# Performance work log

Measured on AMD Instinct MI355X. Metric: run time of the kernel, lower is better.

The kernel has to match this reference:

```python
import jax, jax.numpy as jnp
import numpy as np

N = 4096
W_SCALE = 1.0 / N  # default W_scale = 1/N


def setup_inputs() -> dict:
    key = jax.random.key(0)
    k1, k2 = jax.random.split(key)
    # W: (channels=1, H=512, N=4096), randn * 1/N (default W_scale)
    W = jax.random.normal(k1, (1, 512, N), dtype=jnp.float32) * W_SCALE
    # Lambda_im: omega init -> 2*pi*n/N mod 2*pi; uniform [0, 2pi) stand-in
    Lambda_im = jax.random.uniform(k2, (N,), dtype=jnp.float32) * (2.0 * np.pi)
    return {"W": W, "Lambda_im": Lambda_im, "L": 8192}


def reference(W, Lambda_im, L):
    # version='Lambda_imag_W_real', kernel_to_real='real':
    # K[c,h,l] = sum_n W[c,h,n] * cos(Lambda_im[n] * l)
    pos = jnp.arange(L, dtype=jnp.float32)          # (L,)
    S = jnp.cos(Lambda_im[:, None] * pos[None, :])  # (N, L) Vandermonde-cosine
    K = jnp.einsum("chn,nl->chl", W, S)             # (C, H, L)
    return K
```

## Files before the change

### kernel.cpp

```cpp
#include <hip/hip_runtime.h>
#include <hip/hip_bf16.h>
#include <math.h>


typedef __bf16 bf16_t;
typedef bf16_t bf16x8 __attribute__((ext_vector_type(8)));
typedef float f32x16 __attribute__((ext_vector_type(16)));

#define NK 4096
#define LO 8192
#define BM 128
#define BN 128
#define BK 32
#define LDK 40

__device__ __forceinline__ uint32_t cvt_pk(float lo, float hi) {
    uint32_t r;
    asm("v_cvt_pk_bf16_f32 %0, %1, %2" : "=v"(r) : "v"(lo), "v"(hi));
    return r;
}

__global__ __launch_bounds__(256) void dlr_cosgemm(
    const float* __restrict__ W,
    const float* __restrict__ Lam,
    float* __restrict__ out)
{
    __shared__ uint32_t tbl[NK];
    __shared__ float    cheb[NK];
    __shared__ bf16_t   Al[2][BM][LDK];
    __shared__ bf16_t   Sl[2][BN][LDK];

    const int tid = threadIdx.x;
    const int bid = blockIdx.x;
    const int mt = (bid >> 1) & 3;
    const int nt = ((bid >> 3) << 1) | (bid & 1);
    const int m0 = mt * BM;
    const int n0 = nt * BN;

    for (int i = tid; i < NK; i += 256) {
        double mu = (double)Lam[i] * 0.15915494309189535;
        int a = (int)rint(mu * 8192.0);
        double eps = mu - (double)a * (1.0 / 8192.0);
        int e = (int)rint(eps * 536870912.0);
        e = e > 32767 ? 32767 : (e < -32768 ? -32768 : e);
        tbl[i] = ((uint32_t)a << 16) | ((uint32_t)e & 0xffffu);
        double fr = mu - rint(mu);
        cheb[i] = 2.0f * __builtin_amdgcn_cosf((float)fr);
    }

    const int skk  = (tid & 15) * 2;
    const int srow = (tid >> 4) * 8;
    const int sl0  = n0 + srow;
    const float l29 = (float)sl0 * 0x1p-29f;

    const int arow = tid >> 1;
    const int akh  = (tid & 1) * 16;
    const float* aptr = W + (size_t)(m0 + arow) * NK + akh;

    const int wid = tid >> 6;
    const int lane = tid & 63;
    const int wm = (wid >> 1) * 64;
    const int wn = (wid & 1) * 64;
    const int r31 = lane & 31;
    const int hi8 = (lane >> 5) * 8;

    f32x16 acc[2][2];
    #pragma unroll
    for (int i = 0; i < 2; ++i)
        #pragma unroll
        for (int j = 0; j < 2; ++j)
            #pragma unroll
            for (int r = 0; r < 16; ++r)
                acc[i][j][r] = 0.f;

    __syncthreads();

    auto chain8 = [&](int k, float* c) {
        uint32_t pk = tbl[k];
        float c2 = cheb[k];
        float ef = (float)(int)(short)(pk & 0xffffu);
        uint32_t a = pk >> 16;
        uint32_t prod = a * (uint32_t)sl0;
        float f0 = fmaf((float)(prod & 8191u), 0x1p-13f, ef * l29);
        f0 -= rintf(f0);
        float mu = fmaf((float)a, 0x1p-13f, ef * 0x1p-29f);
        float f1 = f0 + mu; f1 -= rintf(f1);
        c[0] = __builtin_amdgcn_cosf(f0);
        c[1] = __builtin_amdgcn_cosf(f1);
        #pragma unroll
        for (int j = 2; j < 8; ++j) c[j] = fmaf(c2, c[j - 1], -c[j - 2]);
    };

    auto stageS = [&](int buf, int k0) {
        float ca[8], cb[8];
        chain8(k0 + skk, ca);
        chain8(k0 + skk + 1, cb);
        #pragma unroll
        for (int j = 0; j < 8; ++j)
            *(uint32_t*)&Sl[buf][srow + j][skk] = cvt_pk(ca[j], cb[j]);
    };

    auto stageA = [&](int buf, int k0) {
        const float4* g = (const float4*)(aptr + k0);
        float4 v0 = g[0], v1 = g[1], v2 = g[2], v3 = g[3];
        uint4 q0, q1;
        q0.x = cvt_pk(v0.x, v0.y); q0.y = cvt_pk(v0.z, v0.w);
        q0.z = cvt_pk(v1.x, v1.y); q0.w = cvt_pk(v1.z, v1.w);
        q1.x = cvt_pk(v2.x, v2.y); q1.y = cvt_pk(v2.z, v2.w);
        q1.z = cvt_pk(v3.x, v3.y); q1.w = cvt_pk(v3.z, v3.w);
        *(uint4*)&Al[buf][arow][akh]     = q0;
        *(uint4*)&Al[buf][arow][akh + 8] = q1;
    };

    auto compute = [&](int buf) {
        #pragma unroll
        for (int ks = 0; ks < 2; ++ks) {
            const int ko = ks * 16 + hi8;
            bf16x8 a0 = *(const bf16x8*)&Al[buf][wm + r31][ko];
            bf16x8 a1 = *(const bf16x8*)&Al[buf][wm + 32 + r31][ko];
            bf16x8 b0 = *(const bf16x8*)&Sl[buf][wn + r31][ko];
            bf16x8 b1 = *(const bf16x8*)&Sl[buf][wn + 32 + r31][ko];
            acc[0][0] = __builtin_amdgcn_mfma_f32_32x32x16_bf16(a0, b0, acc[0][0], 0, 0, 0);
            acc[0][1] = __builtin_amdgcn_mfma_f32_32x32x16_bf16(a0, b1, acc[0][1], 0, 0, 0);
            acc[1][0] = __builtin_amdgcn_mfma_f32_32x32x16_bf16(a1, b0, acc[1][0], 0, 0, 0);
            acc[1][1] = __builtin_amdgcn_mfma_f32_32x32x16_bf16(a1, b1, acc[1][1], 0, 0, 0);
        }
    };

    stageA(0, 0);
    stageS(0, 0);
    __syncthreads();

    #pragma unroll 2
    for (int it = 0; it < 127; ++it) {
        const int cur = it & 1;
        stageA(cur ^ 1, (it + 1) * BK);
        stageS(cur ^ 1, (it + 1) * BK);
        compute(cur);
        __syncthreads();
    }
    compute(1);

    #pragma unroll
    for (int mi = 0; mi < 2; ++mi) {
        #pragma unroll
        for (int ni = 0; ni < 2; ++ni) {
            const int col = n0 + wn + ni * 32 + r31;
            const int rbase = m0 + wm + mi * 32 + 4 * (lane >> 5);
            #pragma unroll
            for (int reg = 0; reg < 16; ++reg) {
                const int row = rbase + (reg & 3) + 8 * (reg >> 2);
                out[(size_t)row * LO + col] = acc[mi][ni][reg];
            }
        }
    }
}

extern "C" void kernel_launch(void* const* d_in, const int* in_sizes, int n_in,
                              void* d_out, int out_size, void* d_ws, size_t ws_size,
                              hipStream_t stream) {
    const float* W = (const float*)d_in[0];
    const float* Lam = (const float*)d_in[1];
    float* out = (float*)d_out;
    dlr_cosgemm<<<dim3(256), dim3(256), 0, stream>>>(W, Lam, out);
}
```

Measured before the change: 157.0 us.

## Split into prep kernel and split-K 512-thread main GEMM with global A fragments

A prep kernel computes the frequency table and Chebyshev coefficients once and converts W to bf16 in workspace. The main kernel uses 512 threads with an intra-block split-K across two wave groups, BK raised to 64, and A fragments loaded directly from global bf16 into registers with prefetch. Partial sums are reduced through shared memory. This removes the redundant per-block table setup and the A staging through LDS, at the cost of an extra launch, workspace traffic and a reduction epilogue. The original single kernel is kept as a fallback when the workspace is too small.

```diff
diff --git a/kernel.cpp b/kernel.cpp
--- a/kernel.cpp
+++ b/kernel.cpp
@@ -8,11 +8,12 @@
 typedef float f32x16 __attribute__((ext_vector_type(16)));
 
 #define NK 4096
+#define MH 512
 #define LO 8192
 #define BM 128
 #define BN 128
-#define BK 32
-#define LDK 40
+#define BK 64
+#define LDK 72
 
 __device__ __forceinline__ uint32_t cvt_pk(float lo, float hi) {
     uint32_t r;
@@ -20,15 +21,197 @@
     return r;
 }
 
-__global__ __launch_bounds__(256) void dlr_cosgemm(
-    const float* __restrict__ W,
-    const float* __restrict__ Lam,
-    float* __restrict__ out)
+__global__ __launch_bounds__(256) void dlr_prep(
+    const float* __restrict__ W, const float* __restrict__ Lam, void* __restrict__ ws)
+{
+    uint32_t* tbl  = (uint32_t*)ws;
+    float*    cheb = (float*)((char*)ws + NK * 4);
+    bf16_t*   Wb   = (bf16_t*)((char*)ws + NK * 8);
+    const int gid = blockIdx.x * 256 + threadIdx.x;
+    if (gid < NK) {
+        double mu = (double)Lam[gid] * 0.15915494309189535;
+        int a = (int)rint(mu * 8192.0);
+        double eps = mu - (double)a * (1.0 / 8192.0);
+        int e = (int)rint(eps * 536870912.0);
+        e = e > 32767 ? 32767 : (e < -32768 ? -32768 : e);
+        tbl[gid] = ((uint32_t)a << 16) | ((uint32_t)e & 0xffffu);
+        double fr = mu - rint(mu);
+        cheb[gid] = 2.0f * __builtin_amdgcn_cosf((float)fr);
+    }
+    size_t base = (size_t)gid * 8;
+    if (base < (size_t)MH * NK) {
+        const float4* s = (const float4*)(W + base);
+        float4 v0 = s[0], v1 = s[1];
+        uint4 q;
+        q.x = cvt_pk(v0.x, v0.y); q.y = cvt_pk(v0.z, v0.w);
+        q.z = cvt_pk(v1.x, v1.y); q.w = cvt_pk(v1.z, v1.w);
+        *(uint4*)(Wb + base) = q;
+    }
+}
+
+__global__ __launch_bounds__(512, 2) void dlr_main(
+    const void* __restrict__ ws, float* __restrict__ out)
+{
+    const uint32_t* tbl  = (const uint32_t*)ws;
+    const float*    cheb = (const float*)((const char*)ws + NK * 4);
+    const bf16_t*   Wb   = (const bf16_t*)((const char*)ws + NK * 8);
+
+    __shared__ bf16_t Sl[2][BN][LDK];
+    __shared__ float  red[BM][BN + 2];
+
+    const int tid = threadIdx.x;
+    const int bid = blockIdx.x;
+    const int mt = (bid >> 1) & 3;
+    const int nt = ((bid >> 3) << 1) | (bid & 1);
+    const int m0 = mt * BM;
+    const int n0 = nt * BN;
+
+    const int skk  = (tid & 31) * 2;
+    const int srow = (tid >> 5) * 8;
+    const int sl0  = n0 + srow;
+    const float l29 = (float)sl0 * 0x1p-29f;
+
+    const int wid  = tid >> 6;
+    const int lane = tid & 63;
+    const int kg   = wid & 1;
+    const int wn   = ((wid >> 1) & 1) * 64;
+    const int wm   = ((wid >> 2) & 1) * 64;
+    const int r31  = lane & 31;
+    const int hi8  = (lane >> 5) * 8;
+
+    const bf16_t* abase[2][2];
+    #pragma unroll
+    for (int mi = 0; mi < 2; ++mi)
+        #pragma unroll
+        for (int ks = 0; ks < 2; ++ks)
+            abase[mi][ks] = Wb + (size_t)(m0 + wm + mi * 32 + r31) * NK
+                               + kg * 32 + ks * 16 + hi8;
+
+    f32x16 acc[2][2];
+    #pragma unroll
+    for (int i = 0; i < 2; ++i)
+        #pragma unroll
+        for (int j = 0; j < 2; ++j)
+            #pragma unroll
+            for (int r = 0; r < 16; ++r)
+                acc[i][j][r] = 0.f;
+
+    uint32_t tA, tB; float cA, cB;
+    auto loadTbl = [&](int t) {
+        int k = t * BK + skk;
+        tA = tbl[k]; tB = tbl[k + 1];
+        cA = cheb[k]; cB = cheb[k + 1];
+    };
+
+    auto chain8 = [&](uint32_t pk, float c2, float* c) {
+        float ef = (float)(int)(short)(pk & 0xffffu);
+        uint32_t a = pk >> 16;
+        uint32_t prod = a * (uint32_t)sl0;
+        float f0 = fmaf((float)(prod & 8191u), 0x1p-13f, ef * l29);
+        f0 -= rintf(f0);
+        float mu = fmaf((float)a, 0x1p-13f, ef * 0x1p-29f);
+        float f1 = f0 + mu; f1 -= rintf(f1);
+        c[0] = __builtin_amdgcn_cosf(f0);
+        c[1] = __builtin_amdgcn_cosf(f1);
+        #pragma unroll
+        for (int j = 2; j < 8; ++j) c[j] = fmaf(c2, c[j - 1], -c[j - 2]);
+    };
+
+    auto stageS = [&](int buf) {
+        float ca[8], cb[8];
+        chain8(tA, cA, ca);
+        chain8(tB, cB, cb);
+        #pragma unroll
+        for (int j = 0; j < 8; ++j)
+            *(uint32_t*)&Sl[buf][srow + j][skk] = cvt_pk(ca[j], cb[j]);
+    };
+
+    bf16x8 aCur[2][2], aNxt[2][2];
+    auto loadA = [&](bf16x8 a[2][2], int it) {
+        #pragma unroll
+        for (int mi = 0; mi < 2; ++mi)
+            #pragma unroll
+            for (int ks = 0; ks < 2; ++ks)
+                a[mi][ks] = *(const bf16x8*)(abase[mi][ks] + (size_t)it * BK);
+    };
+
+    auto compute = [&](int buf, bf16x8 a[2][2]) {
+        bf16x8 bfr[2][2];
+        #pragma unroll
+        for (int ks = 0; ks < 2; ++ks)
+            #pragma unroll
+            for (int ni = 0; ni < 2; ++ni)
+                bfr[ni][ks] = *(const bf16x8*)&Sl[buf][wn + ni * 32 + r31]
+                                                 [kg * 32 + ks * 16 + hi8];
+        #pragma unroll
+        for (int ks = 0; ks < 2; ++ks)
+            #pragma unroll
+            for (int mi = 0; mi < 2; ++mi)
+                #pragma unroll
+                for (int ni = 0; ni < 2; ++ni)
+                    acc[mi][ni] = __builtin_amdgcn_mfma_f32_32x32x16_bf16(
+                        a[mi][ks], bfr[ni][ks], acc[mi][ni], 0, 0, 0);
+    };
+
+    loadTbl(0);
+    loadA(aCur, 0);
+    stageS(0);
+    loadTbl(1);
+    loadA(aNxt, 0);
+    __syncthreads();
+
+    #pragma unroll 2
+    for (int it = 0; it < 64; ++it) {
+        const int cur = it & 1;
+        if (it < 63) {
+            loadA(aNxt, it + 1);
+            stageS(cur ^ 1);
+        }
+        if (it < 62) loadTbl(it + 2);
+        compute(cur, aCur);
+        #pragma unroll
+        for (int mi = 0; mi < 2; ++mi)
+            #pragma unroll
+            for (int ks = 0; ks < 2; ++ks)
+                aCur[mi][ks] = aNxt[mi][ks];
+        __syncthreads();
+    }
+
+    if (kg == 1) {
+        #pragma unroll
+        for (int mi = 0; mi < 2; ++mi)
+            #pragma unroll
+            for (int ni = 0; ni < 2; ++ni)
+                #pragma unroll
+                for (int rr = 0; rr < 16; ++rr) {
+                    const int row = wm + mi * 32 + (rr & 3) + 8 * (rr >> 2) + 4 * (lane >> 5);
+                    red[row][wn + ni * 32 + r31] = acc[mi][ni][rr];
+                }
+    }
+    __syncthreads();
+    if (kg == 0) {
+        #pragma unroll
+        for (int mi = 0; mi < 2; ++mi)
+            #pragma unroll
+            for (int ni = 0; ni < 2; ++ni) {
+                const int col = n0 + wn + ni * 32 + r31;
+                #pragma unroll
+                for (int rr = 0; rr < 16; ++rr) {
+                    const int row = wm + mi * 32 + (rr & 3) + 8 * (rr >> 2) + 4 * (lane >> 5);
+                    out[(size_t)(m0 + row) * LO + col] =
+                        acc[mi][ni][rr] + red[row][wn + ni * 32 + r31];
+                }
+            }
+    }
+}
+
+__global__ __launch_bounds__(256) void dlr_fb(
+    const float* __restrict__ W, const float* __restrict__ Lam, float* __restrict__ out)
 {
     __shared__ uint32_t tbl[NK];
     __shared__ float    cheb[NK];
-    __shared__ bf16_t   Al[2][BM][LDK];
-    __shared__ bf16_t   Sl[2][BN][LDK];
+    __shared__ bf16_t   Al[2][BM][40];
+    __shared__ bf16_t   Slf[2][BN][40];
 
     const int tid = threadIdx.x;
     const int bid = blockIdx.x;
@@ -52,11 +235,9 @@
     const int srow = (tid >> 4) * 8;
     const int sl0  = n0 + srow;
     const float l29 = (float)sl0 * 0x1p-29f;
-
     const int arow = tid >> 1;
     const int akh  = (tid & 1) * 16;
     const float* aptr = W + (size_t)(m0 + arow) * NK + akh;
-
     const int wid = tid >> 6;
     const int lane = tid & 63;
     const int wm = (wid >> 1) * 64;
@@ -70,9 +251,7 @@
         #pragma unroll
         for (int j = 0; j < 2; ++j)
             #pragma unroll
-            for (int r = 0; r < 16; ++r)
-                acc[i][j][r] = 0.f;
-
+            for (int r = 0; r < 16; ++r) acc[i][j][r] = 0.f;
     __syncthreads();
 
     auto chain8 = [&](int k, float* c) {
@@ -90,16 +269,14 @@
         #pragma unroll
         for (int j = 2; j < 8; ++j) c[j] = fmaf(c2, c[j - 1], -c[j - 2]);
     };
-
     auto stageS = [&](int buf, int k0) {
         float ca[8], cb[8];
         chain8(k0 + skk, ca);
         chain8(k0 + skk + 1, cb);
         #pragma unroll
         for (int j = 0; j < 8; ++j)
-            *(uint32_t*)&Sl[buf][srow + j][skk] = cvt_pk(ca[j], cb[j]);
-    };
-
+            *(uint32_t*)&Slf[buf][srow + j][skk] = cvt_pk(ca[j], cb[j]);
+    };
     auto stageA = [&](int buf, int k0) {
         const float4* g = (const float4*)(aptr + k0);
         float4 v0 = g[0], v1 = g[1], v2 = g[2], v3 = g[3];
@@ -111,15 +288,14 @@
         *(uint4*)&Al[buf][arow][akh]     = q0;
         *(uint4*)&Al[buf][arow][akh + 8] = q1;
     };
-
     auto compute = [&](int buf) {
         #pragma unroll
         for (int ks = 0; ks < 2; ++ks) {
             const int ko = ks * 16 + hi8;
             bf16x8 a0 = *(const bf16x8*)&Al[buf][wm + r31][ko];
             bf16x8 a1 = *(const bf16x8*)&Al[buf][wm + 32 + r31][ko];
-            bf16x8 b0 = *(const bf16x8*)&Sl[buf][wn + r31][ko];
-            bf16x8 b1 = *(const bf16x8*)&Sl[buf][wn + 32 + r31][ko];
+            bf16x8 b0 = *(const bf16x8*)&Slf[buf][wn + r31][ko];
+            bf16x8 b1 = *(const bf16x8*)&Slf[buf][wn + 32 + r31][ko];
             acc[0][0] = __builtin_amdgcn_mfma_f32_32x32x16_bf16(a0, b0, acc[0][0], 0, 0, 0);
             acc[0][1] = __builtin_amdgcn_mfma_f32_32x32x16_bf16(a0, b1, acc[0][1], 0, 0, 0);
             acc[1][0] = __builtin_amdgcn_mfma_f32_32x32x16_bf16(a1, b0, acc[1][0], 0, 0, 0);
@@ -130,19 +306,18 @@
     stageA(0, 0);
     stageS(0, 0);
     __syncthreads();
-
     #pragma unroll 2
     for (int it = 0; it < 127; ++it) {
         const int cur = it & 1;
-        stageA(cur ^ 1, (it + 1) * BK);
-        stageS(cur ^ 1, (it + 1) * BK);
+        stageA(cur ^ 1, (it + 1) * 32);
+        stageS(cur ^ 1, (it + 1) * 32);
         compute(cur);
         __syncthreads();
     }
     compute(1);
 
     #pragma unroll
-    for (int mi = 0; mi < 2; ++mi) {
+    for (int mi = 0; mi < 2; ++mi)
         #pragma unroll
         for (int ni = 0; ni < 2; ++ni) {
             const int col = n0 + wn + ni * 32 + r31;
@@ -153,7 +328,6 @@
                 out[(size_t)row * LO + col] = acc[mi][ni][reg];
             }
         }
-    }
 }
 
 extern "C" void kernel_launch(void* const* d_in, const int* in_sizes, int n_in,
@@ -162,5 +336,11 @@
     const float* W = (const float*)d_in[0];
     const float* Lam = (const float*)d_in[1];
     float* out = (float*)d_out;
-    dlr_cosgemm<<<dim3(256), dim3(256), 0, stream>>>(W, Lam, out);
-}
+    const size_t need = (size_t)NK * 8 + (size_t)MH * NK * 2;
+    if (ws_size >= need) {
+        dlr_prep<<<dim3(1024), dim3(256), 0, stream>>>(W, Lam, d_ws);
+        dlr_main<<<dim3(256), dim3(512), 0, stream>>>(d_ws, out);
+    } else {
+        dlr_fb<<<dim3(256), dim3(256), 0, stream>>>(W, Lam, out);
+    }
+}
```

Result: faster. 132.8 us (-15.4%).

## Split block into producer waves generating cosine tiles and consumer MFMA waves

Applied to the files above, without the earlier changes.

Doubles the block to 512 threads. Four producer waves compute the Chebyshev cosine S-tile into shared memory, while four consumer waves load W directly from global memory into registers, convert it to bf16 and run the MFMAs. BK grows to 64, the A shared-memory tile is removed, A is register-prefetched one step ahead, and s_setprio is raised around the MFMA block. The aim is to overlap the transcendental and VALU work of S generation with matrix-core work. In exchange, each thread holds more registers, and W reads from global memory are strided across rows per lane.

```diff
diff --git a/kernel.cpp b/kernel.cpp
--- a/kernel.cpp
+++ b/kernel.cpp
@@ -8,11 +8,12 @@
 typedef float f32x16 __attribute__((ext_vector_type(16)));
 
 #define NK 4096
+#define MH 512
 #define LO 8192
 #define BM 128
 #define BN 128
-#define BK 32
-#define LDK 40
+#define BK 64
+#define LDK 72
 
 __device__ __forceinline__ uint32_t cvt_pk(float lo, float hi) {
     uint32_t r;
@@ -20,14 +21,13 @@
     return r;
 }
 
-__global__ __launch_bounds__(256) void dlr_cosgemm(
+__global__ __launch_bounds__(512, 2) void dlr_pc(
     const float* __restrict__ W,
     const float* __restrict__ Lam,
     float* __restrict__ out)
 {
     __shared__ uint32_t tbl[NK];
     __shared__ float    cheb[NK];
-    __shared__ bf16_t   Al[2][BM][LDK];
     __shared__ bf16_t   Sl[2][BN][LDK];
 
     const int tid = threadIdx.x;
@@ -37,7 +37,7 @@
     const int m0 = mt * BM;
     const int n0 = nt * BN;
 
-    for (int i = tid; i < NK; i += 256) {
+    for (int i = tid; i < NK; i += 512) {
         double mu = (double)Lam[i] * 0.15915494309189535;
         int a = (int)rint(mu * 8192.0);
         double eps = mu - (double)a * (1.0 / 8192.0);
@@ -48,21 +48,48 @@
         cheb[i] = 2.0f * __builtin_amdgcn_cosf((float)fr);
     }
 
-    const int skk  = (tid & 15) * 2;
-    const int srow = (tid >> 4) * 8;
+    const int wid  = tid >> 6;
+    const int lane = tid & 63;
+    const bool producer = (wid < 4);
+
+    const int skk  = (tid & 31) * 2;
+    const int srow = ((tid >> 5) & 7) * 16;
     const int sl0  = n0 + srow;
     const float l29 = (float)sl0 * 0x1p-29f;
 
-    const int arow = tid >> 1;
-    const int akh  = (tid & 1) * 16;
-    const float* aptr = W + (size_t)(m0 + arow) * NK + akh;
+    auto chain16 = [&](uint32_t pk, float c2, float* c) {
+        float ef = (float)(int)(short)(pk & 0xffffu);
+        uint32_t a = pk >> 16;
+        uint32_t prod = a * (uint32_t)sl0;
+        float f0 = fmaf((float)(prod & 8191u), 0x1p-13f, ef * l29);
+        f0 -= rintf(f0);
+        float mu = fmaf((float)a, 0x1p-13f, ef * 0x1p-29f);
+        float f1 = f0 + mu; f1 -= rintf(f1);
+        c[0] = __builtin_amdgcn_cosf(f0);
+        c[1] = __builtin_amdgcn_cosf(f1);
+        #pragma unroll
+        for (int j = 2; j < 16; ++j) c[j] = fmaf(c2, c[j - 1], -c[j - 2]);
+    };
 
-    const int wid = tid >> 6;
-    const int lane = tid & 63;
-    const int wm = (wid >> 1) * 64;
-    const int wn = (wid & 1) * 64;
+    auto stageS = [&](int buf, int k0) {
+        const int k = k0 + skk;
+        uint32_t pkA = tbl[k], pkB = tbl[k + 1];
+        float cA = cheb[k], cB = cheb[k + 1];
+        float ca[16], cb[16];
+        chain16(pkA, cA, ca);
+        chain16(pkB, cB, cb);
+        #pragma unroll
+        for (int j = 0; j < 16; ++j)
+            *(uint32_t*)&Sl[buf][srow + j][skk] = cvt_pk(ca[j], cb[j]);
+    };
+
+    const int cw  = wid - 4;
+    const int wm  = ((cw >> 1) & 1) * 64;
+    const int wn  = (cw & 1) * 64;
     const int r31 = lane & 31;
     const int hi8 = (lane >> 5) * 8;
+    const float* arow0 = W + (size_t)(m0 + wm + r31) * NK;
+    const float* arow1 = W + (size_t)(m0 + wm + 32 + r31) * NK;
 
     f32x16 acc[2][2];
     #pragma unroll
@@ -73,86 +100,80 @@
             for (int r = 0; r < 16; ++r)
                 acc[i][j][r] = 0.f;
 
-    __syncthreads();
+    float4 pfA[2][8], pfB[2][8];
 
-    auto chain8 = [&](int k, float* c) {
-        uint32_t pk = tbl[k];
-        float c2 = cheb[k];
-        float ef = (float)(int)(short)(pk & 0xffffu);
-        uint32_t a = pk >> 16;
-        uint32_t prod = a * (uint32_t)sl0;
-        float f0 = fmaf((float)(prod & 8191u), 0x1p-13f, ef * l29);
-        f0 -= rintf(f0);
-        float mu = fmaf((float)a, 0x1p-13f, ef * 0x1p-29f);
-        float f1 = f0 + mu; f1 -= rintf(f1);
-        c[0] = __builtin_amdgcn_cosf(f0);
-        c[1] = __builtin_amdgcn_cosf(f1);
+    auto loadA = [&](float4 (&pf)[2][8], int it) {
         #pragma unroll
-        for (int j = 2; j < 8; ++j) c[j] = fmaf(c2, c[j - 1], -c[j - 2]);
-    };
-
-    auto stageS = [&](int buf, int k0) {
-        float ca[8], cb[8];
-        chain8(k0 + skk, ca);
-        chain8(k0 + skk + 1, cb);
-        #pragma unroll
-        for (int j = 0; j < 8; ++j)
-            *(uint32_t*)&Sl[buf][srow + j][skk] = cvt_pk(ca[j], cb[j]);
-    };
-
-    auto stageA = [&](int buf, int k0) {
-        const float4* g = (const float4*)(aptr + k0);
-        float4 v0 = g[0], v1 = g[1], v2 = g[2], v3 = g[3];
-        uint4 q0, q1;
-        q0.x = cvt_pk(v0.x, v0.y); q0.y = cvt_pk(v0.z, v0.w);
-        q0.z = cvt_pk(v1.x, v1.y); q0.w = cvt_pk(v1.z, v1.w);
-        q1.x = cvt_pk(v2.x, v2.y); q1.y = cvt_pk(v2.z, v2.w);
-        q1.z = cvt_pk(v3.x, v3.y); q1.w = cvt_pk(v3.z, v3.w);
-        *(uint4*)&Al[buf][arow][akh]     = q0;
-        *(uint4*)&Al[buf][arow][akh + 8] = q1;
-    };
-
-    auto compute = [&](int buf) {
-        #pragma unroll
-        for (int ks = 0; ks < 2; ++ks) {
-            const int ko = ks * 16 + hi8;
-            bf16x8 a0 = *(const bf16x8*)&Al[buf][wm + r31][ko];
-            bf16x8 a1 = *(const bf16x8*)&Al[buf][wm + 32 + r31][ko];
-            bf16x8 b0 = *(const bf16x8*)&Sl[buf][wn + r31][ko];
-            bf16x8 b1 = *(const bf16x8*)&Sl[buf][wn + 32 + r31][ko];
-            acc[0][0] = __builtin_amdgcn_mfma_f32_32x32x16_bf16(a0, b0, acc[0][0], 0, 0, 0);
-            acc[0][1] = __builtin_amdgcn_mfma_f32_32x32x16_bf16(a0, b1, acc[0][1], 0, 0, 0);
-            acc[1][0] = __builtin_amdgcn_mfma_f32_32x32x16_bf16(a1, b0, acc[1][0], 0, 0, 0);
-            acc[1][1] = __builtin_amdgcn_mfma_f32_32x32x16_bf16(a1, b1, acc[1][1], 0, 0, 0);
+        for (int mi = 0; mi < 2; ++mi) {
+            const float4* b = (const float4*)(mi ? arow1 : arow0) + it * 16 + (hi8 >> 2);
+            #pragma unroll
+            for (int ks = 0; ks < 4; ++ks) {
+                pf[mi][ks * 2]     = b[ks * 4];
+                pf[mi][ks * 2 + 1] = b[ks * 4 + 1];
+            }
         }
     };
 
-    stageA(0, 0);
-    stageS(0, 0);
+    auto consume = [&](int buf, float4 (&pin)[2][8], float4 (&pout)[2][8], int nextIt) {
+        bf16x8 af[2][4];
+        #pragma unroll
+        for (int mi = 0; mi < 2; ++mi)
+            #pragma unroll
+            for (int ks = 0; ks < 4; ++ks) {
+                float4 p0 = pin[mi][ks * 2], p1 = pin[mi][ks * 2 + 1];
+                union { uint4 q; bf16x8 v; } w;
+                w.q.x = cvt_pk(p0.x, p0.y); w.q.y = cvt_pk(p0.z, p0.w);
+                w.q.z = cvt_pk(p1.x, p1.y); w.q.w = cvt_pk(p1.z, p1.w);
+                af[mi][ks] = w.v;
+            }
+        loadA(pout, nextIt > 63 ? 63 : nextIt);
+        bf16x8 bfr[2][4];
+        #pragma unroll
+        for (int ni = 0; ni < 2; ++ni)
+            #pragma unroll
+            for (int ks = 0; ks < 4; ++ks)
+                bfr[ni][ks] = *(const bf16x8*)&Sl[buf][wn + ni * 32 + r31][ks * 16 + hi8];
+        __builtin_amdgcn_s_setprio(1);
+        #pragma unroll
+        for (int ks = 0; ks < 4; ++ks)
+            #pragma unroll
+            for (int mi = 0; mi < 2; ++mi)
+                #pragma unroll
+                for (int ni = 0; ni < 2; ++ni)
+                    acc[mi][ni] = __builtin_amdgcn_mfma_f32_32x32x16_bf16(
+                        af[mi][ks], bfr[ni][ks], acc[mi][ni], 0, 0, 0);
+        __builtin_amdgcn_s_setprio(0);
+    };
+
     __syncthreads();
 
-    #pragma unroll 2
-    for (int it = 0; it < 127; ++it) {
-        const int cur = it & 1;
-        stageA(cur ^ 1, (it + 1) * BK);
-        stageS(cur ^ 1, (it + 1) * BK);
-        compute(cur);
+    if (producer) stageS(0, 0);
+    else          loadA(pfA, 0);
+    __syncthreads();
+
+    for (int it2 = 0; it2 < 32; ++it2) {
+        const int it = it2 * 2;
+        if (producer) stageS(1, (it + 1) * BK);
+        else          consume(0, pfA, pfB, it + 1);
+        __syncthreads();
+        if (producer) { if (it + 1 < 63) stageS(0, (it + 2) * BK); }
+        else          consume(1, pfB, pfA, it + 2);
         __syncthreads();
     }
-    compute(1);
 
-    #pragma unroll
-    for (int mi = 0; mi < 2; ++mi) {
+    if (!producer) {
         #pragma unroll
-        for (int ni = 0; ni < 2; ++ni) {
-            const int col = n0 + wn + ni * 32 + r31;
-            const int rbase = m0 + wm + mi * 32 + 4 * (lane >> 5);
+        for (int mi = 0; mi < 2; ++mi)
             #pragma unroll
-            for (int reg = 0; reg < 16; ++reg) {
-                const int row = rbase + (reg & 3) + 8 * (reg >> 2);
-                out[(size_t)row * LO + col] = acc[mi][ni][reg];
+            for (int ni = 0; ni < 2; ++ni) {
+                const int col = n0 + wn + ni * 32 + r31;
+                const int rbase = m0 + wm + mi * 32 + 4 * (lane >> 5);
+                #pragma unroll
+                for (int rr = 0; rr < 16; ++rr) {
+                    const int row = rbase + (rr & 3) + 8 * (rr >> 2);
+                    out[(size_t)row * LO + col] = acc[mi][ni][rr];
+                }
             }
-        }
     }
 }
 
@@ -162,5 +183,5 @@
     const float* W = (const float*)d_in[0];
     const float* Lam = (const float*)d_in[1];
     float* out = (float*)d_out;
-    dlr_cosgemm<<<dim3(256), dim3(256), 0, stream>>>(W, Lam, out);
+    dlr_pc<<<dim3(256), dim3(512), 0, stream>>>(W, Lam, out);
 }
```

After: 243.5 us. 1.55x slower.
